# Kernel optimization log

Measured on AMD Instinct MI355X. Metric: run time of the kernel, lower is better.

The kernel has to match this reference:

```python
import jax, jax.numpy as jnp
import numpy as np

B, S, D, T = 32, 2048, 128, 8  # batch, seq, input_size, num_trans


def setup_inputs() -> dict:
    key = jax.random.key(0)
    k0, k1, k2, k3 = jax.random.split(key, 4)
    return {
        "input_data": jax.random.normal(k0, (B, S, D), dtype=jnp.float32),
        # nn.Linear(D, D) weights per transform, stacked: [T, D, D]
        "Wx": jax.random.normal(k1, (T, D, D), dtype=jnp.float32) / np.sqrt(D).astype(np.float32),
        "bx": jax.random.normal(k2, (T, D), dtype=jnp.float32) * 0.01,
        # torch.rand init in original
        "p_vectors": jax.random.uniform(k3, (T, 1, D), dtype=jnp.float32),
    }


def reference(input_data, Wx, bx, p_vectors):
    # Batched version of the Python loop of per-transform Linears.
    # torch Linear computes x @ W.T + b -> contract last dim of x with last dim of W.
    transformed = jnp.einsum('bsd,ted->tbse', input_data, Wx) + bx[:, None, None, :]  # [T,B,S,D]

    # Cosine-similarity gating against prototype vectors p_vectors [T,1,D].
    x_norm = jnp.linalg.norm(input_data, axis=2, keepdims=True)[None]        # [1,B,S,1]
    p_norm = jnp.linalg.norm(p_vectors, axis=2, keepdims=True)[:, None]      # [T,1,1,1]
    dot = jnp.sum(input_data[None] * p_vectors[:, None], axis=3, keepdims=True)  # [T,B,S,1]
    cos = dot / (x_norm * p_norm)
    sim = jax.nn.softmax(cos, axis=0)  # softmax over the T transforms

    # Weighted combine + residual (is_y=False path).
    return jnp.sum(sim * transformed, axis=0) + input_data  # [B,S,D]
```

## Files before the change

kernel.cpp:

```cpp
#include <hip/hip_runtime.h>

#define Bq 32
#define Sq 2048
#define Dq 128
#define Tq 8
#define Mq (Bq * Sq)

typedef __attribute__((ext_vector_type(8))) short bf16x8;
typedef __attribute__((ext_vector_type(4))) float f32x4;

static __device__ __forceinline__ unsigned short f2bf(float f) {
    unsigned int u = __float_as_uint(f);
    unsigned int r = (u + 0x7FFFu + ((u >> 16) & 1u)) >> 16;
    return (unsigned short)r;
}

__global__ void prep_kernel(const float* __restrict__ W, unsigned short* __restrict__ wsw) {
    int i = blockIdx.x * 256 + threadIdx.x;
    int j    = i & 7;
    int lane = (i >> 3) & 63;
    int k    = (i >> 9) & 3;
    int n    = (i >> 11) & 7;
    int t    = i >> 14;
    int e = n * 16 + (lane & 15);
    int d = k * 32 + (lane >> 4) * 8 + j;
    wsw[i] = f2bf(W[(t * 128 + e) * 128 + d]);
}

__global__ __launch_bounds__(256) void sim_kernel(const float* __restrict__ x,
                                                  const float* __restrict__ p,
                                                  float* __restrict__ sim) {
    __shared__ float4 p4[Tq][32];
    __shared__ float  pinv[Tq];
    int tid = threadIdx.x;
    reinterpret_cast<float4*>(&p4[0][0])[tid] = reinterpret_cast<const float4*>(p)[tid];
    __syncthreads();
    if (tid < Tq) {
        float s = 0.f;
        #pragma unroll
        for (int i = 0; i < 32; i++) {
            float4 v = p4[tid][i];
            s += v.x * v.x + v.y * v.y + v.z * v.z + v.w * v.w;
        }
        pinv[tid] = rsqrtf(s);
    }
    __syncthreads();

    int m = blockIdx.x * 256 + tid;
    const float4* xr = reinterpret_cast<const float4*>(x) + (size_t)m * 32;
    float acc[Tq];
    #pragma unroll
    for (int t = 0; t < Tq; t++) acc[t] = 0.f;
    float nrm = 0.f;
    #pragma unroll 4
    for (int i = 0; i < 32; i++) {
        float4 v = xr[i];
        nrm += v.x * v.x + v.y * v.y + v.z * v.z + v.w * v.w;
        #pragma unroll
        for (int t = 0; t < Tq; t++) {
            float4 pv = p4[t][i];
            acc[t] += v.x * pv.x + v.y * pv.y + v.z * pv.z + v.w * pv.w;
        }
    }
    float xinv = rsqrtf(nrm);
    float c[Tq], mx = -1e30f;
    #pragma unroll
    for (int t = 0; t < Tq; t++) {
        c[t] = acc[t] * xinv * pinv[t];
        mx = fmaxf(mx, c[t]);
    }
    float sum = 0.f;
    #pragma unroll
    for (int t = 0; t < Tq; t++) { c[t] = __expf(c[t] - mx); sum += c[t]; }
    float inv = 1.f / sum;
    float* so = sim + (size_t)m * Tq;
    #pragma unroll
    for (int t = 0; t < Tq; t++) so[t] = c[t] * inv;
}

__global__ __launch_bounds__(256, 2) void main_kernel(const float* __restrict__ x,
                                                      const unsigned short* __restrict__ wsw,
                                                      const float* __restrict__ bx,
                                                      const float* __restrict__ simg,
                                                      float* __restrict__ out) {
    __shared__ unsigned short xs[128][136];
    __shared__ float simT[Tq][128];
    __shared__ float bxl[Tq][128];
    int tid = threadIdx.x;
    size_t m0 = (size_t)blockIdx.x * 128;

    const float4* xg4 = reinterpret_cast<const float4*>(x + m0 * 128);
    #pragma unroll
    for (int it = 0; it < 16; it++) {
        int flat = it * 256 + tid;
        int row = flat >> 5;
        int c4  = flat & 31;
        float4 v = xg4[flat];
        ushort4 b;
        b.x = f2bf(v.x); b.y = f2bf(v.y); b.z = f2bf(v.z); b.w = f2bf(v.w);
        *reinterpret_cast<ushort4*>(&xs[row][c4 * 4]) = b;
    }
    {
        float4 sv = reinterpret_cast<const float4*>(simg + m0 * Tq)[tid];
        int mloc = tid >> 1;
        int t0   = (tid & 1) * 4;
        simT[t0 + 0][mloc] = sv.x;
        simT[t0 + 1][mloc] = sv.y;
        simT[t0 + 2][mloc] = sv.z;
        simT[t0 + 3][mloc] = sv.w;
    }
    reinterpret_cast<float4*>(&bxl[0][0])[tid] = reinterpret_cast<const float4*>(bx)[tid];
    __syncthreads();

    int wid  = tid >> 6;
    int lane = tid & 63;
    int l16  = lane & 15;
    int quad = lane >> 4;
    int mrow = (wid >> 1) * 64;
    int ncol = (wid & 1) * 64;

    bf16x8 a[4][4];
    #pragma unroll
    for (int mt = 0; mt < 4; mt++)
        #pragma unroll
        for (int k = 0; k < 4; k++)
            a[mt][k] = *reinterpret_cast<const bf16x8*>(&xs[mrow + mt * 16 + l16][k * 32 + quad * 8]);

    f32x4 o[4][4] = {};

    #pragma unroll 1
    for (int t = 0; t < Tq; t++) {
        f32x4 s[4];
        #pragma unroll
        for (int mt = 0; mt < 4; mt++)
            s[mt] = *reinterpret_cast<const f32x4*>(&simT[t][mrow + mt * 16 + quad * 4]);

        #pragma unroll
        for (int n = 0; n < 4; n++) {
            int nt = (ncol >> 4) + n;
            const bf16x8* bp = reinterpret_cast<const bf16x8*>(wsw) + ((size_t)(t * 8 + nt) * 4) * 64 + lane;
            f32x4 y[4] = {};
            #pragma unroll
            for (int k = 0; k < 4; k++) {
                bf16x8 bfrag = bp[(size_t)k * 64];
                #pragma unroll
                for (int mt = 0; mt < 4; mt++)
                    y[mt] = __builtin_amdgcn_mfma_f32_16x16x32_bf16(a[mt][k], bfrag, y[mt], 0, 0, 0);
            }
            float bias = bxl[t][ncol + n * 16 + l16];
            #pragma unroll
            for (int mt = 0; mt < 4; mt++)
                #pragma unroll
                for (int r = 0; r < 4; r++)
                    o[mt][n][r] += s[mt][r] * (y[mt][r] + bias);
        }
    }

    #pragma unroll
    for (int mt = 0; mt < 4; mt++)
        #pragma unroll
        for (int r = 0; r < 4; r++) {
            size_t row = m0 + mrow + mt * 16 + quad * 4 + r;
            #pragma unroll
            for (int n = 0; n < 4; n++) {
                size_t idx = row * 128 + ncol + n * 16 + l16;
                out[idx] = x[idx] + o[mt][n][r];
            }
        }
}

extern "C" void kernel_launch(void* const* d_in, const int* in_sizes, int n_in,
                              void* d_out, int out_size, void* d_ws, size_t ws_size,
                              hipStream_t stream) {
    const float* x   = (const float*)d_in[0];
    const float* Wx  = (const float*)d_in[1];
    const float* bx  = (const float*)d_in[2];
    const float* p   = (const float*)d_in[3];
    float* out = (float*)d_out;

    unsigned short* wsw = (unsigned short*)d_ws;
    float* simg = (float*)((char*)d_ws + 262144);

    prep_kernel<<<dim3(512), dim3(256), 0, stream>>>(Wx, wsw);
    sim_kernel<<<dim3(Mq / 256), dim3(256), 0, stream>>>(x, p, simg);
    main_kernel<<<dim3(Mq / 128), dim3(256), 0, stream>>>(x, wsw, bx, simg, out);
}
```

Before: 123.2 us.

## Fuse cosine-similarity softmax into main GEMM kernel and double-buffer weight fragments

```diff
diff --git a/kernel.cpp b/kernel.cpp
--- a/kernel.cpp
+++ b/kernel.cpp
@@ -27,13 +27,30 @@
     wsw[i] = f2bf(W[(t * 128 + e) * 128 + d]);
 }
 
-__global__ __launch_bounds__(256) void sim_kernel(const float* __restrict__ x,
-                                                  const float* __restrict__ p,
-                                                  float* __restrict__ sim) {
+__global__ __launch_bounds__(256, 2) void main_kernel(const float* __restrict__ x,
+                                                      const unsigned short* __restrict__ wsw,
+                                                      const float* __restrict__ bx,
+                                                      const float* __restrict__ p,
+                                                      float* __restrict__ out) {
+    __shared__ unsigned short xs[128][136];
+    __shared__ float simT[Tq][128];
+    __shared__ float bxl[Tq][128];
     __shared__ float4 p4[Tq][32];
-    __shared__ float  pinv[Tq];
+    __shared__ float pinv[Tq];
+
     int tid = threadIdx.x;
+    size_t m0 = (size_t)blockIdx.x * 128;
+
+    int r = tid >> 1;
+    int h = tid & 1;
+
+    const float4* xg = reinterpret_cast<const float4*>(x + (m0 + r) * 128) + h * 16;
+    float4 xv[16];
+    #pragma unroll
+    for (int j = 0; j < 16; j++) xv[j] = xg[j];
+
     reinterpret_cast<float4*>(&p4[0][0])[tid] = reinterpret_cast<const float4*>(p)[tid];
+    reinterpret_cast<float4*>(&bxl[0][0])[tid] = reinterpret_cast<const float4*>(bx)[tid];
     __syncthreads();
     if (tid < Tq) {
         float s = 0.f;
@@ -46,70 +63,46 @@
     }
     __syncthreads();
 
-    int m = blockIdx.x * 256 + tid;
-    const float4* xr = reinterpret_cast<const float4*>(x) + (size_t)m * 32;
-    float acc[Tq];
+    float dot[Tq];
     #pragma unroll
-    for (int t = 0; t < Tq; t++) acc[t] = 0.f;
-    float nrm = 0.f;
-    #pragma unroll 4
-    for (int i = 0; i < 32; i++) {
-        float4 v = xr[i];
-        nrm += v.x * v.x + v.y * v.y + v.z * v.z + v.w * v.w;
+    for (int t = 0; t < Tq; t++) dot[t] = 0.f;
+    float ssq = 0.f;
+    #pragma unroll
+    for (int j = 0; j < 16; j++) {
+        float4 v = xv[j];
+        ssq += v.x * v.x + v.y * v.y + v.z * v.z + v.w * v.w;
         #pragma unroll
         for (int t = 0; t < Tq; t++) {
-            float4 pv = p4[t][i];
-            acc[t] += v.x * pv.x + v.y * pv.y + v.z * pv.z + v.w * pv.w;
+            float4 pv = p4[t][h * 16 + j];
+            dot[t] += v.x * pv.x + v.y * pv.y + v.z * pv.z + v.w * pv.w;
         }
     }
-    float xinv = rsqrtf(nrm);
+    #pragma unroll
+    for (int jj = 0; jj < 8; jj++) {
+        float4 v0 = xv[2 * jj], v1 = xv[2 * jj + 1];
+        bf16x8 b;
+        b[0] = (short)f2bf(v0.x); b[1] = (short)f2bf(v0.y);
+        b[2] = (short)f2bf(v0.z); b[3] = (short)f2bf(v0.w);
+        b[4] = (short)f2bf(v1.x); b[5] = (short)f2bf(v1.y);
+        b[6] = (short)f2bf(v1.z); b[7] = (short)f2bf(v1.w);
+        *reinterpret_cast<bf16x8*>(&xs[r][h * 64 + jj * 8]) = b;
+    }
+    ssq += __shfl_xor(ssq, 1);
+    #pragma unroll
+    for (int t = 0; t < Tq; t++) dot[t] += __shfl_xor(dot[t], 1);
+    float xinv = rsqrtf(ssq);
     float c[Tq], mx = -1e30f;
     #pragma unroll
     for (int t = 0; t < Tq; t++) {
-        c[t] = acc[t] * xinv * pinv[t];
+        c[t] = dot[t] * xinv * pinv[t];
         mx = fmaxf(mx, c[t]);
     }
     float sum = 0.f;
     #pragma unroll
     for (int t = 0; t < Tq; t++) { c[t] = __expf(c[t] - mx); sum += c[t]; }
     float inv = 1.f / sum;
-    float* so = sim + (size_t)m * Tq;
     #pragma unroll
-    for (int t = 0; t < Tq; t++) so[t] = c[t] * inv;
-}
-
-__global__ __launch_bounds__(256, 2) void main_kernel(const float* __restrict__ x,
-                                                      const unsigned short* __restrict__ wsw,
-                                                      const float* __restrict__ bx,
-                                                      const float* __restrict__ simg,
-                                                      float* __restrict__ out) {
-    __shared__ unsigned short xs[128][136];
-    __shared__ float simT[Tq][128];
-    __shared__ float bxl[Tq][128];
-    int tid = threadIdx.x;
-    size_t m0 = (size_t)blockIdx.x * 128;
-
-    const float4* xg4 = reinterpret_cast<const float4*>(x + m0 * 128);
-    #pragma unroll
-    for (int it = 0; it < 16; it++) {
-        int flat = it * 256 + tid;
-        int row = flat >> 5;
-        int c4  = flat & 31;
-        float4 v = xg4[flat];
-        ushort4 b;
-        b.x = f2bf(v.x); b.y = f2bf(v.y); b.z = f2bf(v.z); b.w = f2bf(v.w);
-        *reinterpret_cast<ushort4*>(&xs[row][c4 * 4]) = b;
-    }
-    {
-        float4 sv = reinterpret_cast<const float4*>(simg + m0 * Tq)[tid];
-        int mloc = tid >> 1;
-        int t0   = (tid & 1) * 4;
-        simT[t0 + 0][mloc] = sv.x;
-        simT[t0 + 1][mloc] = sv.y;
-        simT[t0 + 2][mloc] = sv.z;
-        simT[t0 + 3][mloc] = sv.w;
-    }
-    reinterpret_cast<float4*>(&bxl[0][0])[tid] = reinterpret_cast<const float4*>(bx)[tid];
+    for (int i = 0; i < 4; i++) simT[h * 4 + i][r] = c[h * 4 + i] * inv;
     __syncthreads();
 
     int wid  = tid >> 6;
@@ -118,6 +111,7 @@
     int quad = lane >> 4;
     int mrow = (wid >> 1) * 64;
     int ncol = (wid & 1) * 64;
+    int nt0  = ncol >> 4;
 
     bf16x8 a[4][4];
     #pragma unroll
@@ -128,6 +122,12 @@
 
     f32x4 o[4][4] = {};
 
+    const bf16x8* wbase = reinterpret_cast<const bf16x8*>(wsw);
+    bf16x8 bf[2][4];
+    #pragma unroll
+    for (int k = 0; k < 4; k++)
+        bf[0][k] = wbase[((size_t)(0 * 8 + nt0) * 4 + k) * 64 + lane];
+
     #pragma unroll 1
     for (int t = 0; t < Tq; t++) {
         f32x4 s[4];
@@ -137,34 +137,38 @@
 
         #pragma unroll
         for (int n = 0; n < 4; n++) {
-            int nt = (ncol >> 4) + n;
-            const bf16x8* bp = reinterpret_cast<const bf16x8*>(wsw) + ((size_t)(t * 8 + nt) * 4) * 64 + lane;
+            const int cur = n & 1;
+            {
+                const int n2 = (n + 1) & 3;
+                int t2 = (n == 3) ? ((t + 1) & 7) : t;
+                #pragma unroll
+                for (int k = 0; k < 4; k++)
+                    bf[cur ^ 1][k] = wbase[((size_t)(t2 * 8 + nt0 + n2) * 4 + k) * 64 + lane];
+            }
             f32x4 y[4] = {};
             #pragma unroll
-            for (int k = 0; k < 4; k++) {
-                bf16x8 bfrag = bp[(size_t)k * 64];
+            for (int k = 0; k < 4; k++)
                 #pragma unroll
                 for (int mt = 0; mt < 4; mt++)
-                    y[mt] = __builtin_amdgcn_mfma_f32_16x16x32_bf16(a[mt][k], bfrag, y[mt], 0, 0, 0);
-            }
+                    y[mt] = __builtin_amdgcn_mfma_f32_16x16x32_bf16(a[mt][k], bf[cur][k], y[mt], 0, 0, 0);
             float bias = bxl[t][ncol + n * 16 + l16];
             #pragma unroll
             for (int mt = 0; mt < 4; mt++)
                 #pragma unroll
-                for (int r = 0; r < 4; r++)
-                    o[mt][n][r] += s[mt][r] * (y[mt][r] + bias);
+                for (int rr = 0; rr < 4; rr++)
+                    o[mt][n][rr] += s[mt][rr] * (y[mt][rr] + bias);
         }
     }
 
     #pragma unroll
     for (int mt = 0; mt < 4; mt++)
         #pragma unroll
-        for (int r = 0; r < 4; r++) {
-            size_t row = m0 + mrow + mt * 16 + quad * 4 + r;
+        for (int rr = 0; rr < 4; rr++) {
+            size_t row = m0 + mrow + mt * 16 + quad * 4 + rr;
             #pragma unroll
             for (int n = 0; n < 4; n++) {
                 size_t idx = row * 128 + ncol + n * 16 + l16;
-                out[idx] = x[idx] + o[mt][n][r];
+                out[idx] = x[idx] + o[mt][n][rr];
             }
         }
 }
@@ -179,9 +183,7 @@
     float* out = (float*)d_out;
 
     unsigned short* wsw = (unsigned short*)d_ws;
-    float* simg = (float*)((char*)d_ws + 262144);
 
     prep_kernel<<<dim3(512), dim3(256), 0, stream>>>(Wx, wsw);
-    sim_kernel<<<dim3(Mq / 256), dim3(256), 0, stream>>>(x, p, simg);
-    main_kernel<<<dim3(Mq / 128), dim3(256), 0, stream>>>(x, wsw, bx, simg, out);
+    main_kernel<<<dim3(Mq / 128), dim3(256), 0, stream>>>(x, wsw, bx, p, out);
 }
```

New measurement: 112.3 us. 8.9% less time.
